# Kernel optimization log

Measured on AMD Instinct MI355X. Metric: run time of the kernel, lower is better.

Reference implementation:

```python
import jax, jax.numpy as jnp
import numpy as np


def _l2n(v, eps=1e-12):
    return v / (jnp.linalg.norm(v) + eps)


def _sn(W, u):
    # Spectral normalization with one power-iteration step.
    # W: [Cin, Cout] (1x1 conv kernel flattened), u: [Cin] persistent vector.
    v = _l2n(W.T @ u)            # [Cout]
    u_new = _l2n(W @ v)          # [Cin]
    v = jax.lax.stop_gradient(v)
    u_new = jax.lax.stop_gradient(u_new)
    sigma = u_new @ (W @ v)      # scalar, grads flow through W only
    return W / sigma


def _conv1x1(x, W, b, u):
    # x: [B,H,W,Cin], spectrally-normalized 1x1 conv == GEMM over channels
    return jnp.einsum('bhwc,cd->bhwd', x, _sn(W, u)) + b


def setup_inputs() -> dict:
    key = jax.random.key(0)
    ks = jax.random.split(key, 14)
    B, H, W, C = 8, 64, 64, 256
    Cq = C // 8  # 32
    s = lambda fan_in: 1.0 / np.sqrt(fan_in)
    return {
        'x':  jax.random.normal(ks[0], (B, H, W, C), jnp.float32),
        'Wf': jax.random.normal(ks[1], (C, Cq), jnp.float32) * s(C),
        'bf': jnp.zeros((Cq,), jnp.float32),
        'uf': jax.random.normal(ks[2], (C,), jnp.float32),
        'Wg': jax.random.normal(ks[3], (C, Cq), jnp.float32) * s(C),
        'bg': jnp.zeros((Cq,), jnp.float32),
        'ug': jax.random.normal(ks[4], (C,), jnp.float32),
        'Wh': jax.random.normal(ks[5], (C, C), jnp.float32) * s(C),
        'bh': jnp.zeros((C,), jnp.float32),
        'uh': jax.random.normal(ks[6], (C,), jnp.float32),
        'Wc': jax.random.normal(ks[7], (C, C), jnp.float32) * s(C),
        'bc': jnp.zeros((C,), jnp.float32),
        'uc': jax.random.normal(ks[8], (C,), jnp.float32),
        'gamma': jnp.float32(0.7),  # nonzero so attention branch contributes
    }


def reference(x, Wf, bf, uf, Wg, bg, ug, Wh, bh, uh, Wc, bc, uc, gamma):
    B, H, W, C = x.shape
    N = H * W
    flat = lambda t: t.reshape(B, N, t.shape[-1])
    f = flat(_conv1x1(x, Wf, bf, uf))   # [B,N,C/8] keys
    g = flat(_conv1x1(x, Wg, bg, ug))   # [B,N,C/8] queries
    h = flat(_conv1x1(x, Wh, bh, uh))   # [B,N,C]   values
    s = jnp.einsum('bqd,bkd->bqk', g, f)          # [B,N,N]
    beta = jax.nn.softmax(s, axis=-1)
    o = jnp.einsum('bqk,bkc->bqc', beta, h)       # [B,N,C]
    o = o.reshape(B, H, W, C)
    o = _conv1x1(o, Wc, bc, uc)
    return gamma * o + x
```

## Files before the change

### kernel.cpp

```cpp
#include <hip/hip_runtime.h>

typedef unsigned short ushort_t;
typedef __attribute__((ext_vector_type(8))) __bf16 bf16x8;
typedef __attribute__((ext_vector_type(4))) float f32x4;
typedef __attribute__((ext_vector_type(4))) ushort_t ushort4_t;

__device__ inline ushort_t f2bf(float f){
  __bf16 h = (__bf16)f;
  union { __bf16 h; ushort_t u; } v; v.h = h;
  return v.u;
}

__device__ inline f32x4 mfma16(bf16x8 a, bf16x8 b, f32x4 c){
  return __builtin_amdgcn_mfma_f32_16x16x32_bf16(a, b, c, 0, 0, 0);
}

#define GLDS16(gsrc, ldst) \
  __builtin_amdgcn_global_load_lds((const __attribute__((address_space(1))) unsigned int*)(gsrc), \
                                   (__attribute__((address_space(3))) unsigned int*)(ldst), 16, 0, 0)

__global__ void sigma_kernel(const float* __restrict__ Wf, const float* __restrict__ uf,
                             const float* __restrict__ Wg, const float* __restrict__ ug,
                             const float* __restrict__ Wh, const float* __restrict__ uh,
                             const float* __restrict__ Wc, const float* __restrict__ uc,
                             float* __restrict__ inv_sigma){
  int w = blockIdx.x, t = threadIdx.x;
  const float *W, *u; int Cout;
  if      (w == 0){ W = Wf; u = uf; Cout = 32; }
  else if (w == 1){ W = Wg; u = ug; Cout = 32; }
  else if (w == 2){ W = Wh; u = uh; Cout = 256; }
  else            { W = Wc; u = uc; Cout = 256; }
  __shared__ float su[256], sv[256], red[256];
  su[t] = u[t];
  __syncthreads();
  float v = 0.f;
  if (t < Cout){
    for (int i = 0; i < 256; ++i) v += W[i*Cout + t] * su[i];
  }
  red[t] = (t < Cout) ? v*v : 0.f;
  __syncthreads();
  for (int s = 128; s > 0; s >>= 1){ if (t < s) red[t] += red[t+s]; __syncthreads(); }
  float nv = sqrtf(red[0]) + 1e-12f;
  __syncthreads();
  if (t < Cout) sv[t] = v / nv;
  __syncthreads();
  float wv = 0.f;
  for (int d = 0; d < Cout; ++d) wv += W[t*Cout + d] * sv[d];
  __syncthreads();
  red[t] = wv * wv;
  __syncthreads();
  for (int s = 128; s > 0; s >>= 1){ if (t < s) red[t] += red[t+s]; __syncthreads(); }
  if (t == 0){
    float ss2 = red[0];
    float sig = ss2 / (sqrtf(ss2) + 1e-12f);
    inv_sigma[w] = 1.0f / sig;
  }
}

__global__ void prep_weights(const float* __restrict__ Wf, const float* __restrict__ Wg,
                             const float* __restrict__ Wh, const float* __restrict__ Wc,
                             const float* __restrict__ inv_sigma,
                             ushort_t* __restrict__ WallT, ushort_t* __restrict__ WcT){
  int idx = blockIdx.x * 256 + threadIdx.x;
  if (idx < 81920){
    int c = idx >> 8, k = idx & 255;
    float val, is;
    if (c < 32)      { val = Wf[k*32  + c      ]; is = inv_sigma[0]; }
    else if (c < 64) { val = Wg[k*32  + (c-32) ]; is = inv_sigma[1]; }
    else             { val = Wh[k*256 + (c-64) ]; is = inv_sigma[2]; }
    WallT[idx] = f2bf(val * is);
  } else {
    int j = idx - 81920; int c = j >> 8, k = j & 255;
    WcT[j] = f2bf(Wc[k*256 + c] * inv_sigma[3]);
  }
}

__global__ __launch_bounds__(256) void fgh_kernel(
    const float* __restrict__ x, const ushort_t* __restrict__ WallT,
    const float* __restrict__ bf, const float* __restrict__ bg, const float* __restrict__ bh,
    ushort_t* __restrict__ fO, ushort_t* __restrict__ gO, ushort_t* __restrict__ hT){
  __shared__ __attribute__((aligned(16))) char ldsX[4][16384];
  int t = threadIdx.x;
  int wv = t >> 6, l = t & 63, lrow = l & 15, lgrp = l >> 4;
  long r0 = (long)blockIdx.x * 64 + wv * 16;
  char* ldsW = ldsX[wv];
#pragma unroll
  for (int rloc = 0; rloc < 16; ++rloc){
    const char* src = (const char*)(x + (r0 + rloc)*256)
                    + ((l*16) ^ ((rloc & 7) << 4));
    GLDS16(src, ldsW + rloc*1024);
  }
  asm volatile("s_waitcnt vmcnt(0)" ::: "memory");
  const char* xrow = ldsW + lrow*1024;
  int swzX = (lrow & 7) << 4;
  f32x4 acc[20];
#pragma unroll
  for (int i = 0; i < 20; ++i) acc[i] = f32x4{0.f,0.f,0.f,0.f};
#pragma unroll
  for (int ks = 0; ks < 8; ++ks){
    int bb = ks*128 + lgrp*32;
    f32x4 xa = *(const f32x4*)(xrow + ( bb       ^ swzX));
    f32x4 xb = *(const f32x4*)(xrow + ((bb + 16) ^ swzX));
    union { __bf16 h[8]; bf16x8 v; } A;
#pragma unroll
    for (int j = 0; j < 4; ++j){ A.h[j] = (__bf16)xa[j]; A.h[4+j] = (__bf16)xb[j]; }
    int kk = ks*32 + lgrp*8;
#pragma unroll
    for (int ct = 0; ct < 20; ++ct){
      bf16x8 bbv = *(const bf16x8*)(WallT + (ct*16 + lrow)*256 + kk);
      acc[ct] = mfma16(A.v, bbv, acc[ct]);
    }
  }
#pragma unroll
  for (int ct = 0; ct < 20; ++ct){
    int col = ct*16 + lrow;
    long rowb = r0 + lgrp*4;
    if (col < 32){
      float bv = bf[col];
#pragma unroll
      for (int rg = 0; rg < 4; ++rg) fO[(rowb+rg)*32 + col] = f2bf(acc[ct][rg] + bv);
    } else if (col < 64){
      float bv = bg[col-32];
#pragma unroll
      for (int rg = 0; rg < 4; ++rg)
        gO[(rowb+rg)*32 + (col-32)] = f2bf((acc[ct][rg] + bv) * 1.44269504f);
    } else {
      int hc = col - 64;
      float bv = bh[hc];
      long bb2 = rowb >> 12, n = rowb & 4095;
      int k6 = (int)(n & 63);
      int s6 = (k6 & 32) | (((k6 >> 2) & 3) << 3) | (((k6 >> 4) & 1) << 2) | (k6 & 3);
      long pos = (n & ~63L) | (long)s6;
      ushort4_t pk;
#pragma unroll
      for (int rg = 0; rg < 4; ++rg) pk[rg] = f2bf(acc[ct][rg] + bv);
      *(ushort4_t*)(hT + (bb2*256 + hc)*4096 + pos) = pk;
    }
  }
}

__global__ __launch_bounds__(256, 4) void attn_kernel(
    const ushort_t* __restrict__ fI, const ushort_t* __restrict__ gI,
    const ushort_t* __restrict__ hT,
    ushort_t* __restrict__ oP, float* __restrict__ mP, float* __restrict__ liP){
  __shared__ ushort_t ldsV[256*64];
  int bid = blockIdx.x, t = threadIdx.x;
  int b = bid & 7, rest = bid >> 3, qg = rest >> 1, kh = rest & 1;
  int wv = t >> 6, l = t & 63, lrow = l & 15, lgrp = l >> 4;
  int q0 = qg*64 + wv*16;
  long key_base = (long)kh * 2048;
  bf16x8 qa = *(const bf16x8*)(gI + ((long)b*4096 + q0 + lrow)*32 + lgrp*8);
  const ushort_t* hB = hT + (long)b*256*4096;
  const ushort_t* kp = fI + (long)b*4096*32 + key_base*32 + lrow*32 + lgrp*8;
  const ushort_t* vsrc = hB + (long)(wv*64 + (l>>3))*4096 + key_base
                            + (((l & 7) ^ (l >> 3)) << 3);
  ushort_t* vdst = ldsV + wv*4096;
  f32x4 o[16];
#pragma unroll
  for (int i = 0; i < 16; ++i) o[i] = f32x4{0.f,0.f,0.f,0.f};
  float m = -1e30f, li = 0.f;
  int swzR = (lrow & 7) << 3;
  for (int kt = 0; kt < 32; ++kt){
    __syncthreads();
    bf16x8 kb0 = *(const bf16x8*)(kp);
    bf16x8 kb1 = *(const bf16x8*)(kp + 512);
    bf16x8 kb2 = *(const bf16x8*)(kp + 1024);
    bf16x8 kb3 = *(const bf16x8*)(kp + 1536);
    kp += 2048;
    const ushort_t* vs = vsrc + kt*64;
#pragma unroll
    for (int i = 0; i < 8; ++i)
      GLDS16(vs + i*32768, vdst + i*512);
    f32x4 z = f32x4{0.f,0.f,0.f,0.f};
    f32x4 s0 = mfma16(kb0, qa, z);
    f32x4 s1 = mfma16(kb1, qa, z);
    f32x4 s2 = mfma16(kb2, qa, z);
    f32x4 s3 = mfma16(kb3, qa, z);
    float tm = -1e30f;
#pragma unroll
    for (int rg = 0; rg < 4; ++rg)
      tm = fmaxf(tm, fmaxf(fmaxf(s0[rg], s1[rg]), fmaxf(s2[rg], s3[rg])));
    if (__any(tm > m + 8.f)){
      tm = fmaxf(tm, __shfl_xor(tm, 16));
      tm = fmaxf(tm, __shfl_xor(tm, 32));
      float mn = fmaxf(m, tm);
      float sc = exp2f(m - mn);
      m = mn; li *= sc;
#pragma unroll
      for (int ct = 0; ct < 16; ++ct)
#pragma unroll
        for (int rg = 0; rg < 4; ++rg) o[ct][rg] *= sc;
    }
    union { __bf16 h[8]; bf16x8 v; } pf0, pf1;
#pragma unroll
    for (int rg = 0; rg < 4; ++rg){
      float a0 = exp2f(s0[rg] - m), a1 = exp2f(s1[rg] - m);
      float a2 = exp2f(s2[rg] - m), a3 = exp2f(s3[rg] - m);
      li += (a0 + a1) + (a2 + a3);
      pf0.h[rg] = (__bf16)a0; pf0.h[4+rg] = (__bf16)a1;
      pf1.h[rg] = (__bf16)a2; pf1.h[4+rg] = (__bf16)a3;
    }
    asm volatile("s_waitcnt vmcnt(0)" ::: "memory");
    __syncthreads();
    __builtin_amdgcn_s_setprio(1);
#pragma unroll
    for (int ct = 0; ct < 16; ++ct){
      int base = (ct*16 + lrow) << 6;
      bf16x8 vb0 = *(const bf16x8*)(ldsV + base + (( (lgrp << 3))      ^ swzR));
      bf16x8 vb1 = *(const bf16x8*)(ldsV + base + ((32 + (lgrp << 3)) ^ swzR));
      o[ct] = mfma16(vb0, pf0.v, o[ct]);
      o[ct] = mfma16(vb1, pf1.v, o[ct]);
    }
    __builtin_amdgcn_s_setprio(0);
  }
  li += __shfl_xor(li, 16);
  li += __shfl_xor(li, 32);
  long rbase = (long)b*4096 + q0;
  ushort_t* Ob = oP + ((long)kh*32768 + rbase)*256;
#pragma unroll
  for (int ct = 0; ct < 16; ++ct){
    ushort4_t pk;
#pragma unroll
    for (int rg = 0; rg < 4; ++rg) pk[rg] = f2bf(o[ct][rg]);
    *(ushort4_t*)(Ob + (long)lrow*256 + ct*16 + lgrp*4) = pk;
  }
  if (l < 16){
    mP [kh*32768 + rbase + lrow] = m;
    liP[kh*32768 + rbase + lrow] = li;
  }
}

__global__ __launch_bounds__(256) void out_kernel(
    const ushort_t* __restrict__ oP, const float* __restrict__ mP,
    const float* __restrict__ liP, const ushort_t* __restrict__ WcT,
    const float* __restrict__ bc, const float* __restrict__ x,
    const float* __restrict__ gamma, float* __restrict__ out){
  __shared__ __attribute__((aligned(16))) char ldsO[4][16384];
  int t = threadIdx.x;
  int wv = t >> 6, l = t & 63, lrow = l & 15, lgrp = l >> 4;
  long r0 = (long)blockIdx.x * 64 + wv * 16;
  char* ldsW = ldsO[wv];
#pragma unroll
  for (int i = 0; i < 8; ++i){
    int rloc = 2*i + (l >> 5);
    int soff = ((l & 31)*16) ^ ((rloc & 7) << 4);
    GLDS16((const char*)(oP + (r0 + rloc)*256) + soff,            ldsW + i*1024);
    GLDS16((const char*)(oP + (32768L + r0 + rloc)*256) + soff,   ldsW + 8192 + i*1024);
  }
  long r = r0 + lrow;
  float m1 = mP[r],  m2 = mP[32768 + r];
  float li1 = liP[r], li2 = liP[32768 + r];
  float mm  = fmaxf(m1, m2);
  float sc1 = exp2f(m1 - mm), sc2 = exp2f(m2 - mm);
  float inv = 1.0f / (li1*sc1 + li2*sc2);
  float w1 = sc1 * inv, w2 = sc2 * inv;
  asm volatile("s_waitcnt vmcnt(0)" ::: "memory");
  const char* orow = ldsW + lrow*512;
  int swzO = (lrow & 7) << 4;
  f32x4 acc[16];
#pragma unroll
  for (int i = 0; i < 16; ++i) acc[i] = f32x4{0.f,0.f,0.f,0.f};
#pragma unroll
  for (int ks = 0; ks < 8; ++ks){
    int bb = (ks*64 + lgrp*16) ^ swzO;
    bf16x8 a1 = *(const bf16x8*)(orow + bb);
    bf16x8 a2 = *(const bf16x8*)(orow + 8192 + bb);
    union { __bf16 h[8]; bf16x8 v; } A;
#pragma unroll
    for (int j = 0; j < 8; ++j)
      A.h[j] = (__bf16)((float)a1[j]*w1 + (float)a2[j]*w2);
    int kk = ks*32 + lgrp*8;
#pragma unroll
    for (int ct = 0; ct < 16; ++ct){
      bf16x8 bbv = *(const bf16x8*)(WcT + (ct*16 + lrow)*256 + kk);
      acc[ct] = mfma16(A.v, bbv, acc[ct]);
    }
  }
  float gm = gamma[0];
#pragma unroll
  for (int ct = 0; ct < 16; ++ct){
    int col = ct*16 + lrow;
    float bv = bc[col];
#pragma unroll
    for (int rg = 0; rg < 4; ++rg){
      long row = r0 + lgrp*4 + rg;
      out[row*256 + col] = gm*(acc[ct][rg] + bv) + x[row*256 + col];
    }
  }
}

extern "C" void kernel_launch(void* const* d_in, const int* in_sizes, int n_in,
                              void* d_out, int out_size, void* d_ws, size_t ws_size,
                              hipStream_t stream){
  (void)in_sizes; (void)n_in; (void)out_size; (void)ws_size;
  const float* x  = (const float*)d_in[0];
  const float* Wf = (const float*)d_in[1];
  const float* bf = (const float*)d_in[2];
  const float* uf = (const float*)d_in[3];
  const float* Wg = (const float*)d_in[4];
  const float* bg = (const float*)d_in[5];
  const float* ug = (const float*)d_in[6];
  const float* Wh = (const float*)d_in[7];
  const float* bh = (const float*)d_in[8];
  const float* uh = (const float*)d_in[9];
  const float* Wc = (const float*)d_in[10];
  const float* bc = (const float*)d_in[11];
  const float* uc = (const float*)d_in[12];
  const float* gamma = (const float*)d_in[13];
  float* out = (float*)d_out;

  char* w = (char*)d_ws;
  float*    inv_sigma = (float*)w;
  ushort_t* WallT = (ushort_t*)(w + 256);
  ushort_t* WcT   = (ushort_t*)(w + 164096);
  ushort_t* fW    = (ushort_t*)(w + 295168);
  ushort_t* gW    = (ushort_t*)(w + 2392320);
  ushort_t* hTW   = (ushort_t*)(w + 4489472);
  ushort_t* oPW   = (ushort_t*)(w + 21266688);
  float*    mPW   = (float*)   (w + 54821120);
  float*    liPW  = (float*)   (w + 55083264);

  hipLaunchKernelGGL(sigma_kernel, dim3(4),    dim3(256), 0, stream,
                     Wf, uf, Wg, ug, Wh, uh, Wc, uc, inv_sigma);
  hipLaunchKernelGGL(prep_weights, dim3(576),  dim3(256), 0, stream,
                     Wf, Wg, Wh, Wc, inv_sigma, WallT, WcT);
  hipLaunchKernelGGL(fgh_kernel,   dim3(512),  dim3(256), 0, stream,
                     x, WallT, bf, bg, bh, fW, gW, hTW);
  hipLaunchKernelGGL(attn_kernel,  dim3(1024), dim3(256), 0, stream,
                     fW, gW, hTW, oPW, mPW, liPW);
  hipLaunchKernelGGL(out_kernel,   dim3(512),  dim3(256), 0, stream,
                     oPW, mPW, liPW, WcT, bc, x, gamma, out);
}
```

Before: 216.0 us.

## Split PV work across waves by channel and share probabilities through LDS

In the attention kernel, each wave now computes the output for all 64 queries of the block but only its own 64-channel slice of V. Before, each wave handled 16 queries across all 256 channels. Each wave writes its bf16 probability fragment and its rescale factor to shared memory, and all waves read them back after the barrier. This is meant to cut the per-wave LDS reads of the V tile by a factor of four. In exchange it adds extra LDS stores and loads for P and the scale factors, and a block-wide check on whether any row needs rescaling.

New measurement: 244.1 us. 13.0% more time.

```diff
diff --git a/kernel.cpp b/kernel.cpp
--- a/kernel.cpp
+++ b/kernel.cpp
@@ -144,17 +144,21 @@
     const ushort_t* __restrict__ hT,
     ushort_t* __restrict__ oP, float* __restrict__ mP, float* __restrict__ liP){
   __shared__ ushort_t ldsV[256*64];
+  __shared__ ushort_t ldsP[4*64*16];
+  __shared__ float    ldsSC[64];
   int bid = blockIdx.x, t = threadIdx.x;
   int b = bid & 7, rest = bid >> 3, qg = rest >> 1, kh = rest & 1;
   int wv = t >> 6, l = t & 63, lrow = l & 15, lgrp = l >> 4;
-  int q0 = qg*64 + wv*16;
+  int q0 = qg*64;
   long key_base = (long)kh * 2048;
-  bf16x8 qa = *(const bf16x8*)(gI + ((long)b*4096 + q0 + lrow)*32 + lgrp*8);
+  bf16x8 qa = *(const bf16x8*)(gI + ((long)b*4096 + q0 + wv*16 + lrow)*32 + lgrp*8);
   const ushort_t* hB = hT + (long)b*256*4096;
   const ushort_t* kp = fI + (long)b*4096*32 + key_base*32 + lrow*32 + lgrp*8;
   const ushort_t* vsrc = hB + (long)(wv*64 + (l>>3))*4096 + key_base
                             + (((l & 7) ^ (l >> 3)) << 3);
   ushort_t* vdst = ldsV + wv*4096;
+  int pslot = ((l << 4) ^ ((l & 4) << 3));
+  ushort_t* pw = ldsP + (wv << 10) + pslot;
   f32x4 o[16];
 #pragma unroll
   for (int i = 0; i < 16; ++i) o[i] = f32x4{0.f,0.f,0.f,0.f};
@@ -180,17 +184,15 @@
 #pragma unroll
     for (int rg = 0; rg < 4; ++rg)
       tm = fmaxf(tm, fmaxf(fmaxf(s0[rg], s1[rg]), fmaxf(s2[rg], s3[rg])));
+    float sc_pub = 1.0f;
     if (__any(tm > m + 8.f)){
       tm = fmaxf(tm, __shfl_xor(tm, 16));
       tm = fmaxf(tm, __shfl_xor(tm, 32));
       float mn = fmaxf(m, tm);
-      float sc = exp2f(m - mn);
-      m = mn; li *= sc;
-#pragma unroll
-      for (int ct = 0; ct < 16; ++ct)
-#pragma unroll
-        for (int rg = 0; rg < 4; ++rg) o[ct][rg] *= sc;
-    }
+      sc_pub = exp2f(m - mn);
+      m = mn; li *= sc_pub;
+    }
+    if (l < 16) ldsSC[wv*16 + lrow] = sc_pub;
     union { __bf16 h[8]; bf16x8 v; } pf0, pf1;
 #pragma unroll
     for (int rg = 0; rg < 4; ++rg){
@@ -200,16 +202,41 @@
       pf0.h[rg] = (__bf16)a0; pf0.h[4+rg] = (__bf16)a1;
       pf1.h[rg] = (__bf16)a2; pf1.h[4+rg] = (__bf16)a3;
     }
+    *(bf16x8*)(pw)     = pf0.v;
+    *(bf16x8*)(pw + 8) = pf1.v;
     asm volatile("s_waitcnt vmcnt(0)" ::: "memory");
     __syncthreads();
+    float scq0 = ldsSC[lrow], scq1 = ldsSC[16 + lrow];
+    float scq2 = ldsSC[32 + lrow], scq3 = ldsSC[48 + lrow];
+    if (__any((scq0 != 1.0f) || (scq1 != 1.0f) || (scq2 != 1.0f) || (scq3 != 1.0f))){
+#pragma unroll
+      for (int ct = 0; ct < 4; ++ct)
+#pragma unroll
+        for (int rg = 0; rg < 4; ++rg){
+          o[ct][rg]    *= scq0;
+          o[4+ct][rg]  *= scq1;
+          o[8+ct][rg]  *= scq2;
+          o[12+ct][rg] *= scq3;
+        }
+    }
     __builtin_amdgcn_s_setprio(1);
-#pragma unroll
-    for (int ct = 0; ct < 16; ++ct){
-      int base = (ct*16 + lrow) << 6;
-      bf16x8 vb0 = *(const bf16x8*)(ldsV + base + (( (lgrp << 3))      ^ swzR));
-      bf16x8 vb1 = *(const bf16x8*)(ldsV + base + ((32 + (lgrp << 3)) ^ swzR));
-      o[ct] = mfma16(vb0, pf0.v, o[ct]);
-      o[ct] = mfma16(vb1, pf1.v, o[ct]);
+    bf16x8 vb[8];
+#pragma unroll
+    for (int ct = 0; ct < 4; ++ct){
+      int base = ((wv*64 + ct*16 + lrow) << 6);
+      vb[2*ct]   = *(const bf16x8*)(ldsV + base + (( (lgrp << 3))      ^ swzR));
+      vb[2*ct+1] = *(const bf16x8*)(ldsV + base + ((32 + (lgrp << 3)) ^ swzR));
+    }
+#pragma unroll
+    for (int qt = 0; qt < 4; ++qt){
+      const ushort_t* pr = ldsP + (qt << 10) + pslot;
+      bf16x8 pa0 = *(const bf16x8*)(pr);
+      bf16x8 pa1 = *(const bf16x8*)(pr + 8);
+#pragma unroll
+      for (int ct = 0; ct < 4; ++ct){
+        o[qt*4+ct] = mfma16(vb[2*ct],   pa0, o[qt*4+ct]);
+        o[qt*4+ct] = mfma16(vb[2*ct+1], pa1, o[qt*4+ct]);
+      }
     }
     __builtin_amdgcn_s_setprio(0);
   }
@@ -218,15 +245,17 @@
   long rbase = (long)b*4096 + q0;
   ushort_t* Ob = oP + ((long)kh*32768 + rbase)*256;
 #pragma unroll
-  for (int ct = 0; ct < 16; ++ct){
-    ushort4_t pk;
-#pragma unroll
-    for (int rg = 0; rg < 4; ++rg) pk[rg] = f2bf(o[ct][rg]);
-    *(ushort4_t*)(Ob + (long)lrow*256 + ct*16 + lgrp*4) = pk;
-  }
+  for (int qt = 0; qt < 4; ++qt)
+#pragma unroll
+    for (int ct = 0; ct < 4; ++ct){
+      ushort4_t pk;
+#pragma unroll
+      for (int rg = 0; rg < 4; ++rg) pk[rg] = f2bf(o[qt*4+ct][rg]);
+      *(ushort4_t*)(Ob + (long)(qt*16 + lrow)*256 + wv*64 + ct*16 + lgrp*4) = pk;
+    }
   if (l < 16){
-    mP [kh*32768 + rbase + lrow] = m;
-    liP[kh*32768 + rbase + lrow] = li;
+    mP [kh*32768 + rbase + wv*16 + lrow] = m;
+    liP[kh*32768 + rbase + wv*16 + lrow] = li;
   }
 }
 
```
